# Performance work log

Hardware: AMD Instinct MI355X
Metric: run time of the kernel (lower is better)

Reference implementation:

```python
import jax, jax.numpy as jnp
import numpy as np

BS, Q, S1, S2 = 8, 128, 32, 64
H_DIM, NH = 768, 12
DH = H_DIM // NH


def _linear_params(k, scale=0.02):
    kw, _ = jax.random.split(k)
    w = jax.random.normal(kw, (H_DIM, H_DIM), jnp.float32) * scale
    b = jnp.zeros((H_DIM,), jnp.float32)
    return w, b


def setup_inputs() -> dict:
    root = jax.random.key(0)
    ks = jax.random.split(root, 12)
    wq_w, wq_b = _linear_params(ks[0])
    wk_w, wk_b = _linear_params(ks[1])
    wv_w, wv_b = _linear_params(ks[2])
    sq_w, sq_b = _linear_params(ks[3])
    sk_w, sk_b = _linear_params(ks[4])
    sv_w, sv_b = _linear_params(ks[5])
    return {
        "q_in": jax.random.normal(ks[6], (BS, Q, H_DIM), jnp.float32),
        "k_in": jax.random.normal(ks[7], (BS, S1, S2, H_DIM), jnp.float32),
        "v_in": jax.random.normal(ks[8], (BS, S1, S2, H_DIM), jnp.float32),
        "kvec": jax.random.normal(ks[9], (BS, S1, H_DIM), jnp.float32),
        "word_mask": jnp.ones((BS, S1, S2), jnp.int32),
        "sentence_mask": jnp.ones((BS * Q, S1), jnp.int32),
        "wq_w": wq_w, "wq_b": wq_b, "wk_w": wk_w, "wk_b": wk_b,
        "wv_w": wv_w, "wv_b": wv_b, "sq_w": sq_w, "sq_b": sq_b,
        "sk_w": sk_w, "sk_b": sk_b, "sv_w": sv_w, "sv_b": sv_b,
    }


def reference(q_in, k_in, v_in, kvec, word_mask, sentence_mask,
              wq_w, wq_b, wk_w, wk_b, wv_w, wv_b,
              sq_w, sq_b, sk_w, sk_b, sv_w, sv_b):
    bs, q_len = q_in.shape[0], q_in.shape[1]
    s1, s2 = k_in.shape[1], k_in.shape[2]
    scale = 1.0 / jnp.sqrt(jnp.float32(DH))

    # additive masks, as in the torch module
    wm = (1.0 - word_mask.astype(jnp.float32)) * -10000.0      # [bs, s1, s2]
    sm = (1.0 - sentence_mask.astype(jnp.float32)) * -10000.0  # [bs*Q, s1]

    # ---- word-level attention ----
    q = (q_in @ wq_w + wq_b).reshape(bs, q_len, NH, DH)
    k = (k_in @ wk_w + wk_b).reshape(bs, s1, s2, NH, DH)
    v = (v_in @ wv_w + wv_b).reshape(bs, s1, s2, NH, DH)
    # scores over tokens within each sentence: [bs, s1, H, Q, s2]
    scores1 = jnp.einsum('bqhd,bsthd->bshqt', q, k) * scale
    probs1 = jax.nn.softmax(scores1 + wm[:, :, None, None, :], axis=-1)
    # word_hidden: [bs, Q, s1, h]
    wh = jnp.einsum('bshqt,bsthd->bqshd', probs1, v).reshape(bs, q_len, s1, H_DIM)

    # ---- sentence-level attention ----
    sq = (q_in @ sq_w + sq_b).reshape(bs, q_len, NH, DH)
    sk = (kvec @ sk_w + sk_b).reshape(bs, s1, NH, DH)   # shared across queries
    sv = (wh @ sv_w + sv_b).reshape(bs, q_len, s1, NH, DH)
    scores2 = jnp.einsum('bqhd,bshd->bqhs', sq, sk) * scale  # [bs, Q, H, s1]
    scores2 = scores2 + sm.reshape(bs, q_len, s1)[:, :, None, :]
    probs2 = jax.nn.softmax(scores2, axis=-1)
    out = jnp.einsum('bqhs,bqshd->bqhd', probs2, sv).reshape(bs * q_len, H_DIM)
    return out
```

## Files before the change

### kernel.cpp

```cpp
#include <hip/hip_runtime.h>
#include <hip/hip_bf16.h>


typedef __attribute__((ext_vector_type(8))) short short8;
typedef __attribute__((ext_vector_type(4))) short short4v;
typedef __attribute__((ext_vector_type(4))) float f32x4;

__device__ __forceinline__ short f2bf(float f) {
  __hip_bfloat16 b = __float2bfloat16(f);
  return __builtin_bit_cast(short, b);
}
__device__ __forceinline__ float bf2f(short s) {
  __hip_bfloat16 b = __builtin_bit_cast(__hip_bfloat16, s);
  return __bfloat162float(b);
}

#define MFMA16(a, b, c) __builtin_amdgcn_mfma_f32_16x16x32_bf16((a), (b), (c), 0, 0, 0)

__device__ __forceinline__ void async_load16(const void* g, void* l) {
  auto l3 = (__attribute__((address_space(3))) void*)(uintptr_t)(
      reinterpret_cast<uintptr_t>(l));
  auto g1 = (const __attribute__((address_space(1))) void*)g;
  __builtin_amdgcn_global_load_lds(g1, l3, 16, 0, 0);
}

#define KBAR()                                      \
  do {                                              \
    asm volatile("" ::: "memory");                  \
    __builtin_amdgcn_s_barrier();                   \
    asm volatile("" ::: "memory");                  \
  } while (0)
#define VMW(N) asm volatile("s_waitcnt vmcnt(" #N ")" ::: "memory")

__global__ __launch_bounds__(256)
void prep(const float* __restrict__ w0, const float* __restrict__ w1,
          const float* __restrict__ w2, const float* __restrict__ w3,
          const float* __restrict__ w4, const float* __restrict__ w5,
          short* __restrict__ WT,
          const float* __restrict__ q_in, const float* __restrict__ k_in,
          const float* __restrict__ v_in, const float* __restrict__ kvec,
          short* __restrict__ qbf, short* __restrict__ kbf,
          short* __restrict__ vbf, short* __restrict__ kvb) {
  const int id = blockIdx.x;
  const int tid = threadIdx.x;
  if (id < 3456) {
    __shared__ float tile[32][33];
    const int zz = id / 576, r = id % 576;
    const float* W = (zz == 0) ? w0 : (zz == 1) ? w1 : (zz == 2) ? w2
                   : (zz == 3) ? w3 : (zz == 4) ? w4 : w5;
    short* WTo = WT + (size_t)zz * 768 * 768;
    const int bx = (r % 24) * 32, by = (r / 24) * 32;
    const int tx = tid & 31, ty = tid >> 5;
    #pragma unroll
    for (int i = 0; i < 32; i += 8)
      tile[ty + i][tx] = W[(size_t)(by + ty + i) * 768 + bx + tx];
    __syncthreads();
    #pragma unroll
    for (int i = 0; i < 32; i += 8)
      WTo[(size_t)(bx + ty + i) * 768 + by + tx] = f2bf(tile[tx][ty + i]);
    return;
  }
  const int i = (id - 3456) * 256 + tid;
  const float* src;
  short* dst;
  int idx;
  if (i < 98304)        { src = q_in; dst = qbf; idx = i; }
  else if (i < 1671168) { src = k_in; dst = kbf; idx = i - 98304; }
  else if (i < 3244032) { src = v_in; dst = vbf; idx = i - 1671168; }
  else                  { src = kvec; dst = kvb; idx = i - 3244032; }
  const float4* s = (const float4*)src + (size_t)idx * 2;
  const float4 a = s[0], b = s[1];
  __align__(16) short tmp[8] = {f2bf(a.x), f2bf(a.y), f2bf(a.z), f2bf(a.w),
                                f2bf(b.x), f2bf(b.y), f2bf(b.z), f2bf(b.w)};
  *((short8*)dst + idx) = *(short8*)tmp;
}

__global__ __launch_bounds__(512, 2)
void gemm_proj(const short* __restrict__ kbf, const short* __restrict__ vbf,
               const short* __restrict__ qbf, const short* __restrict__ kvb,
               const short* __restrict__ WT6,
               const float* __restrict__ wk_b, const float* __restrict__ wv_b,
               const float* __restrict__ wq_b, const float* __restrict__ sq_b,
               const float* __restrict__ sk_b,
               short* __restrict__ kp, short* __restrict__ vT,
               short* __restrict__ qp, float* __restrict__ sqp,
               float* __restrict__ skp) {
  const int K = 768, WELEM = 768 * 768;
  extern __shared__ __align__(16) char smem_c[];
  short* smem = (short*)smem_c;
  const int tid = threadIdx.x;
  const int w = tid >> 6, lane = tid & 63, quad = lane >> 4, l16 = lane & 15;
  const f32x4 zero4 = {0.f, 0.f, 0.f, 0.f};

  if (blockIdx.z < 2) {
    short* LA = smem;
    short* LB = smem + 2 * 256 * 64;
    const int z = blockIdx.z;
    const short* Ag = z ? vbf : kbf;
    const short* Bg = z ? (WT6 + 3 * WELEM) : (WT6 + 2 * WELEM);
    const float* bias = z ? wv_b : wk_b;
    const int m0 = blockIdx.x * 256, n0 = blockIdx.y * 256;
    const int wr = w >> 2, wc = w & 3;

    const int srow = lane >> 3;
    const int schk = (lane & 7) ^ srow;
    const short* ag0 = Ag + (size_t)(m0 + w * 8 + srow) * K + schk * 8;
    const short* bg0 = Bg + (size_t)(n0 + w * 8 + srow) * K + schk * 8;
    short* la0 = LA + (w * 8) * 64;
    short* lb0 = LB + (w * 8) * 64;
    const int fsw = l16 & 7;

    f32x4 acc[8][4];
    #pragma unroll
    for (int i = 0; i < 8; i++)
      #pragma unroll
      for (int j = 0; j < 4; j++) acc[i][j] = zero4;

    auto STG1 = [&](int op, int h, int kt) {
      if (kt >= 12) kt -= 2;
      const int buf = kt & 1;
      const short* g = (op ? bg0 : ag0) + (size_t)h * 128 * K + (size_t)kt * 64;
      short* lb = (op ? lb0 : la0) + buf * 16384 + h * (128 * 64);
      async_load16(g, lb);
      async_load16(g + (size_t)64 * K, lb + 64 * 64);
    };

    short8 af[4][2];
    short8 bf2[2][2];

#define LDA_(BUF, IH)                                                        \
  _Pragma("unroll") for (int i = 0; i < 4; i++)                              \
    _Pragma("unroll") for (int kb = 0; kb < 2; kb++)                         \
      af[i][kb] = *(const short8*)&LA[(BUF)*16384 +                          \
          (wr * 128 + (IH)*64 + i * 16 + l16) * 64 +                         \
          (((kb * 4 + quad) ^ fsw) * 8)];
#define LDB_(BUF, JH)                                                        \
  _Pragma("unroll") for (int j = 0; j < 2; j++)                              \
    _Pragma("unroll") for (int kb = 0; kb < 2; kb++)                         \
      bf2[j][kb] = *(const short8*)&LB[(BUF)*16384 +                         \
          (wc * 64 + (JH)*32 + j * 16 + l16) * 64 +                          \
          (((kb * 4 + quad) ^ fsw) * 8)];
#define MM_(IH, JH)                                                          \
  __builtin_amdgcn_s_setprio(1);                                             \
  _Pragma("unroll") for (int i = 0; i < 4; i++)                              \
    _Pragma("unroll") for (int j = 0; j < 2; j++) {                          \
      acc[(IH)*4 + i][(JH)*2 + j] =                                          \
          MFMA16(af[i][0], bf2[j][0], acc[(IH)*4 + i][(JH)*2 + j]);          \
      acc[(IH)*4 + i][(JH)*2 + j] =                                          \
          MFMA16(af[i][1], bf2[j][1], acc[(IH)*4 + i][(JH)*2 + j]);          \
    }                                                                        \
  __builtin_amdgcn_s_setprio(0);

    STG1(0, 0, 0); STG1(0, 1, 0); STG1(1, 0, 0); STG1(1, 1, 0);
    STG1(0, 0, 1);
    VMW(2);
    KBAR();

    #pragma unroll 1
    for (int it = 0; it < 6; ++it) {
      const int kb_t = 2 * it + 1, kc = 2 * it + 2, kd = 2 * it + 3;
      LDA_(0, 0); LDB_(0, 0); STG1(0, 1, kb_t); KBAR(); MM_(0, 0); KBAR();
      LDB_(0, 1); STG1(1, 0, kb_t); KBAR(); MM_(0, 1); KBAR();
      LDA_(0, 1); LDB_(0, 0); STG1(1, 1, kb_t); KBAR(); MM_(1, 0); KBAR();
      LDB_(0, 1); STG1(0, 0, kc); KBAR(); MM_(1, 1); VMW(2); KBAR();
      LDA_(1, 0); LDB_(1, 0); STG1(0, 1, kc); KBAR(); MM_(0, 0); KBAR();
      LDB_(1, 1); STG1(1, 0, kc); KBAR(); MM_(0, 1); KBAR();
      LDA_(1, 1); LDB_(1, 0); STG1(1, 1, kc); KBAR(); MM_(1, 0); KBAR();
      LDB_(1, 1); STG1(0, 0, kd); KBAR(); MM_(1, 1); VMW(2); KBAR();
    }
#undef LDA_
#undef LDB_
#undef MM_

    if (z == 0) {
      #pragma unroll
      for (int I = 0; I < 8; I++)
        #pragma unroll
        for (int J = 0; J < 4; J++) {
          const int col = n0 + wc * 64 + J * 16 + l16;
          const float bv = bias[col];
          #pragma unroll
          for (int r = 0; r < 4; r++) {
            const int g = m0 + wr * 128 + I * 16 + quad * 4 + r;
            kp[(size_t)g * 768 + col] = f2bf(acc[I][J][r] + bv);
          }
        }
    } else {
      const int hh = (n0 >> 6) + wc;
      #pragma unroll
      for (int I = 0; I < 8; I++) {
        const int bs_ = (m0 >> 6) + wr * 2 + (I >> 2);
        const int t0 = (I & 3) * 16 + quad * 4;
        #pragma unroll
        for (int J = 0; J < 4; J++) {
          const int dd = J * 16 + l16;
          const float bv = bias[hh * 64 + dd];
          __align__(8) short tmp[4];
          #pragma unroll
          for (int r = 0; r < 4; r++) tmp[r] = f2bf(acc[I][J][r] + bv);
          *(short4v*)&vT[(((size_t)bs_ * 12 + hh) * 64 + dd) * 64 + t0] =
              *(short4v*)tmp;
        }
      }
    }
    return;
  }

  {
    const int id = blockIdx.x + 64 * blockIdx.y;
    if (id >= 108) return;
    short* As = smem;
    short* Bs = smem + 128 * 32;
    const int qmode = (id < 96);
    const int r = qmode ? id : (id - 96);
    const int bx = qmode ? (r % 8) : (r % 2);
    const int by = qmode ? (r / 8) : (r / 2);
    const short* A = qmode ? qbf : kvb;
    const short* WT = qmode ? (WT6 + 0 * WELEM) : (WT6 + 4 * WELEM);

    const int wm = (w >> 1) * 64, wn = (w & 1) * 64;
    const int m0 = bx * 128, n0 = by * 128;
    const int grow = w * 32 + (lane >> 2);
    const int kc = (lane & 3) * 8;
    const short* ag = A + (size_t)(m0 + grow) * K + kc;
    const short* bg = WT + (size_t)(n0 + grow) * K + kc;
    short* al = &As[(w * 32) * 32];
    short* bl = &Bs[(w * 32) * 32];

    f32x4 acc[4][4];
    #pragma unroll
    for (int i = 0; i < 4; i++)
      #pragma unroll
      for (int j = 0; j < 4; j++) acc[i][j] = zero4;

    for (int k0 = 0; k0 < K; k0 += 32) {
      __syncthreads();
      if (tid < 256) {
        async_load16(ag, al);
        async_load16(ag + (size_t)16 * K, al + 16 * 32);
        async_load16(bg, bl);
        async_load16(bg + (size_t)16 * K, bl + 16 * 32);
      }
      ag += 32;
      bg += 32;
      __syncthreads();
      if (tid < 256) {
        short8 af[4], bf[4];
        #pragma unroll
        for (int i = 0; i < 4; i++)
          af[i] = *(short8*)&As[(wm + i * 16 + l16) * 32 + quad * 8];
        #pragma unroll
        for (int j = 0; j < 4; j++)
          bf[j] = *(short8*)&Bs[(wn + j * 16 + l16) * 32 + quad * 8];
        #pragma unroll
        for (int i = 0; i < 4; i++)
          #pragma unroll
          for (int j = 0; j < 4; j++)
            acc[i][j] = MFMA16(af[i], bf[j], acc[i][j]);
      }
    }
    if (tid >= 256) return;

    #pragma unroll
    for (int i = 0; i < 4; i++) {
      #pragma unroll
      for (int j = 0; j < 4; j++) {
        const int col = n0 + wn + j * 16 + l16;
        const float bv = qmode ? ((col < 768) ? wq_b[col] : sq_b[col - 768])
                               : sk_b[col];
        #pragma unroll
        for (int r4 = 0; r4 < 4; r4++) {
          const int g = m0 + wm + i * 16 + quad * 4 + r4;
          const float v = acc[i][j][r4] + bv;
          if (qmode) {
            if (col < 768) qp[(size_t)g * 768 + col] = f2bf(v * 0.125f);
            else sqp[(size_t)g * 768 + (col - 768)] = v;
          } else {
            skp[(size_t)g * 768 + col] = v;
          }
        }
      }
    }
  }
}

__global__ __launch_bounds__(256)
void wattn_sp(const short* __restrict__ q_proj, const short* __restrict__ k_proj,
              const short* __restrict__ vT, const int* __restrict__ word_mask,
              const float* __restrict__ sq, const float* __restrict__ sk,
              const int* __restrict__ sent_mask, short* __restrict__ wh,
              float* __restrict__ probs2) {
  __shared__ __align__(16) short KVs[128 * 72];
  __shared__ __align__(16) short Ps[128 * 72];
  const int bid = blockIdx.x;
  const int tid = threadIdx.x;

  if (bid >= 3072) {
    float* sc = (float*)KVs;
    const int bq = bid - 3072;
    const int b = bq >> 7, q = bq & 127;
    for (int p = tid; p < 384; p += 256) {
      const int hh = p >> 5, ss = p & 31;
      const float4* a = (const float4*)(sq + ((size_t)(b * 128 + q)) * 768 + hh * 64);
      const float4* c = (const float4*)(sk + ((size_t)(b * 32 + ss)) * 768 + hh * 64);
      float d = 0.f;
      #pragma unroll
      for (int i = 0; i < 16; i++) {
        const float4 av = a[i], cv = c[i];
        d += av.x * cv.x + av.y * cv.y + av.z * cv.z + av.w * cv.w;
      }
      d = d * 0.125f + (1.0f - (float)sent_mask[bq * 32 + ss]) * -10000.0f;
      sc[hh * 33 + ss] = d;
    }
    __syncthreads();
    if (tid < 12) {
      float mx = -3.0e38f;
      for (int ss = 0; ss < 32; ss++) mx = fmaxf(mx, sc[tid * 33 + ss]);
      float sum = 0.f;
      for (int ss = 0; ss < 32; ss++) {
        const float e = __expf(sc[tid * 33 + ss] - mx);
        sc[tid * 33 + ss] = e;
        sum += e;
      }
      const float inv = 1.0f / sum;
      for (int ss = 0; ss < 32; ss++) sc[tid * 33 + ss] *= inv;
    }
    __syncthreads();
    for (int p = tid; p < 384; p += 256) {
      const int hh = p >> 5, ss = p & 31;
      probs2[((size_t)bq * 12 + hh) * 32 + ss] = sc[hh * 33 + ss];
    }
    return;
  }

  short* Ks = KVs;
  short* Vs = KVs + 64 * 72;
  short* Os = KVs;
  const int h = bid % 12, s = (bid / 12) % 32, b = bid / (12 * 32);
  const int w = tid >> 6, lane = tid & 63, quad = lane >> 4, l16 = lane & 15;
  const f32x4 zero4 = {0.f, 0.f, 0.f, 0.f};

  {
    const int t2 = tid & 127;
    const int row8 = t2 >> 3;
    const int c8 = (t2 & 7) * 8;
    if (tid < 128) {
      const short* src = k_proj + ((size_t)((b * 32 + s) * 64)) * 768 + h * 64 + c8;
      #pragma unroll
      for (int i = 0; i < 4; i++) {
        const int r = row8 + i * 16;
        *(short8*)&Ks[r * 72 + c8] = *(const short8*)(src + (size_t)r * 768);
      }
    } else {
      const short* src = vT + ((size_t)((b * 32 + s) * 12 + h)) * 4096 + c8;
      #pragma unroll
      for (int i = 0; i < 4; i++) {
        const int r = row8 + i * 16;
        *(short8*)&Vs[r * 72 + c8] = *(const short8*)(src + (size_t)r * 64);
      }
    }
  }
  __syncthreads();

  f32x4 sac[2][4];
  #pragma unroll
  for (int i = 0; i < 2; i++)
    #pragma unroll
    for (int j = 0; j < 4; j++) sac[i][j] = zero4;
  {
    short8 aq[2][2], bk[4][2];
    #pragma unroll
    for (int i = 0; i < 2; i++)
      #pragma unroll
      for (int kb = 0; kb < 2; kb++)
        aq[i][kb] = *(const short8*)(q_proj +
            ((size_t)(b * 128 + w * 32 + i * 16 + l16)) * 768 + h * 64 + kb * 32 + quad * 8);
    #pragma unroll
    for (int j = 0; j < 4; j++)
      #pragma unroll
      for (int kb = 0; kb < 2; kb++)
        bk[j][kb] = *(short8*)&Ks[(j * 16 + l16) * 72 + kb * 32 + quad * 8];
    #pragma unroll
    for (int i = 0; i < 2; i++)
      #pragma unroll
      for (int j = 0; j < 4; j++) {
        sac[i][j] = MFMA16(aq[i][0], bk[j][0], sac[i][j]);
        sac[i][j] = MFMA16(aq[i][1], bk[j][1], sac[i][j]);
      }
  }

  {
    float wmv[4];
    const int* wmp = word_mask + (b * 32 + s) * 64;
    #pragma unroll
    for (int j = 0; j < 4; j++)
      wmv[j] = (1.0f - (float)wmp[j * 16 + l16]) * -10000.0f;
    #pragma unroll
    for (int i = 0; i < 2; i++) {
      #pragma unroll
      for (int r = 0; r < 4; r++) {
        float vv[4];
        float sum = 0.f;
        #pragma unroll
        for (int j = 0; j < 4; j++) {
          vv[j] = __expf(sac[i][j][r] + wmv[j]);
          sum += vv[j];
        }
        sum += __shfl_xor(sum, 1);
        sum += __shfl_xor(sum, 2);
        sum += __shfl_xor(sum, 4);
        sum += __shfl_xor(sum, 8);
        const float inv = 1.0f / sum;
        const int row = w * 32 + i * 16 + quad * 4 + r;
        #pragma unroll
        for (int j = 0; j < 4; j++)
          Ps[row * 72 + j * 16 + l16] = f2bf(vv[j] * inv);
      }
    }
  }
  __syncthreads();

  f32x4 oac[2][4];
  #pragma unroll
  for (int i = 0; i < 2; i++)
    #pragma unroll
    for (int j = 0; j < 4; j++) oac[i][j] = zero4;
  {
    short8 ap[2][2], bv[4][2];
    #pragma unroll
    for (int i = 0; i < 2; i++)
      #pragma unroll
      for (int kb = 0; kb < 2; kb++)
        ap[i][kb] = *(short8*)&Ps[(w * 32 + i * 16 + l16) * 72 + kb * 32 + quad * 8];
    #pragma unroll
    for (int j = 0; j < 4; j++)
      #pragma unroll
      for (int kb = 0; kb < 2; kb++)
        bv[j][kb] = *(short8*)&Vs[(j * 16 + l16) * 72 + kb * 32 + quad * 8];
    #pragma unroll
    for (int i = 0; i < 2; i++)
      #pragma unroll
      for (int j = 0; j < 4; j++) {
        oac[i][j] = MFMA16(ap[i][0], bv[j][0], oac[i][j]);
        oac[i][j] = MFMA16(ap[i][1], bv[j][1], oac[i][j]);
      }
  }
  __syncthreads();
  #pragma unroll
  for (int i = 0; i < 2; i++)
    #pragma unroll
    for (int j = 0; j < 4; j++)
      #pragma unroll
      for (int r = 0; r < 4; r++)
        Os[(w * 32 + i * 16 + quad * 4 + r) * 72 + j * 16 + l16] = f2bf(oac[i][j][r]);
  __syncthreads();

  {
    const int c8 = (tid & 7) * 8;
    #pragma unroll
    for (int i = 0; i < 4; i++) {
      const int row = i * 32 + (tid >> 3);
      short* dst = wh + (((size_t)(b * 128 + row)) * 32 + s) * 768 + h * 64;
      *(short8*)(dst + c8) = *(const short8*)&Os[row * 72 + c8];
    }
  }
}

__global__ __launch_bounds__(256)
void whc_kernel(const short* __restrict__ wh, const float* __restrict__ probs2,
                short* __restrict__ whc) {
  __shared__ __align__(16) short whs[32 * 776];
  __shared__ float p2s[384];
  const int bq = blockIdx.x, tid = threadIdx.x;
  const short8* src = (const short8*)(wh + (size_t)bq * 24576);
  for (int t = tid; t < 3072; t += 256) {
    const int row = t / 96, c8 = (t % 96) * 8;
    *(short8*)&whs[row * 776 + c8] = src[t];
  }
  for (int p = tid; p < 384; p += 256) p2s[p] = probs2[(size_t)bq * 384 + p];
  __syncthreads();

  float acc[3][12];
  #pragma unroll
  for (int kk = 0; kk < 3; kk++)
    #pragma unroll
    for (int h = 0; h < 12; h++) acc[kk][h] = 0.f;

  for (int s = 0; s < 32; s++) {
    float p2r[12];
    #pragma unroll
    for (int h = 0; h < 12; h++) p2r[h] = p2s[h * 32 + s];
    #pragma unroll
    for (int kk = 0; kk < 3; kk++) {
      const float wv = bf2f(whs[s * 776 + kk * 256 + tid]);
      #pragma unroll
      for (int h = 0; h < 12; h++) acc[kk][h] += p2r[h] * wv;
    }
  }
  #pragma unroll
  for (int h = 0; h < 12; h++)
    #pragma unroll
    for (int kk = 0; kk < 3; kk++)
      whc[((size_t)h * 1024 + bq) * 768 + kk * 256 + tid] = f2bf(acc[kk][h]);
}

__global__ __launch_bounds__(256)
void outg(const short* __restrict__ whc, const short* __restrict__ WTsv,
          const float* __restrict__ sv_b, float* __restrict__ out) {
  const int K = 768;
  __shared__ __align__(16) short As[128 * 32];
  __shared__ __align__(16) short Bs[64 * 32];
  const int tid = threadIdx.x;
  const int m0 = blockIdx.x * 128, h = blockIdx.y;
  const int w = tid >> 6, lane = tid & 63, quad = lane >> 4, l16 = lane & 15;
  const int wm = (w >> 1) * 64, wn = (w & 1) * 32;

  const int grow = w * 32 + (lane >> 2);
  const int kc = (lane & 3) * 8;
  const short* ag = whc + ((size_t)h * 1024 + m0 + grow) * K + kc;
  short* al = &As[(w * 32) * 32];
  const int growb = w * 16 + (lane >> 2);
  const short* bg = WTsv + (size_t)(h * 64 + growb) * K + kc;
  short* bl = &Bs[(w * 16) * 32];

  const f32x4 zero4 = {0.f, 0.f, 0.f, 0.f};
  f32x4 acc[4][2];
  #pragma unroll
  for (int i = 0; i < 4; i++)
    #pragma unroll
    for (int j = 0; j < 2; j++) acc[i][j] = zero4;

  for (int k0 = 0; k0 < K; k0 += 32) {
    __syncthreads();
    async_load16(ag, al);
    async_load16(ag + (size_t)16 * K, al + 16 * 32);
    async_load16(bg, bl);
    ag += 32;
    bg += 32;
    __syncthreads();
    short8 af[4], bf[2];
    #pragma unroll
    for (int i = 0; i < 4; i++)
      af[i] = *(short8*)&As[(wm + i * 16 + l16) * 32 + quad * 8];
    #pragma unroll
    for (int j = 0; j < 2; j++)
      bf[j] = *(short8*)&Bs[(wn + j * 16 + l16) * 32 + quad * 8];
    #pragma unroll
    for (int i = 0; i < 4; i++)
      #pragma unroll
      for (int j = 0; j < 2; j++)
        acc[i][j] = MFMA16(af[i], bf[j], acc[i][j]);
  }

  #pragma unroll
  for (int i = 0; i < 4; i++) {
    #pragma unroll
    for (int j = 0; j < 2; j++) {
      const int col = h * 64 + wn + j * 16 + l16;
      const float bv = sv_b[col];
      #pragma unroll
      for (int r = 0; r < 4; r++) {
        const int g = m0 + wm + i * 16 + quad * 4 + r;
        out[(size_t)g * 768 + col] = acc[i][j][r] + bv;
      }
    }
  }
}

extern "C" void kernel_launch(void* const* d_in, const int* in_sizes, int n_in,
                              void* d_out, int out_size, void* d_ws, size_t ws_size,
                              hipStream_t stream) {
  (void)in_sizes; (void)n_in; (void)out_size; (void)ws_size;
  const float* q_in      = (const float*)d_in[0];
  const float* k_in      = (const float*)d_in[1];
  const float* v_in      = (const float*)d_in[2];
  const float* kvec      = (const float*)d_in[3];
  const int*   word_mask = (const int*)d_in[4];
  const int*   sent_mask = (const int*)d_in[5];
  const float* wq_w = (const float*)d_in[6],  *wq_b = (const float*)d_in[7];
  const float* wk_w = (const float*)d_in[8],  *wk_b = (const float*)d_in[9];
  const float* wv_w = (const float*)d_in[10], *wv_b = (const float*)d_in[11];
  const float* sq_w = (const float*)d_in[12], *sq_b = (const float*)d_in[13];
  const float* sk_w = (const float*)d_in[14], *sk_b = (const float*)d_in[15];
  const float* sv_w = (const float*)d_in[16], *sv_b = (const float*)d_in[17];
  float* out = (float*)d_out;

  const int WELEM = 768 * 768;

  static bool s_attr_done = false;
  if (!s_attr_done) {
    (void)hipFuncSetAttribute(reinterpret_cast<const void*>(&gemm_proj),
                              hipFuncAttributeMaxDynamicSharedMemorySize, 131072);
    s_attr_done = true;
  }

  char* ws = (char*)d_ws;
  size_t off = 0;
  auto alloc = [&](size_t bytes) -> void* {
    void* p = ws + off;
    off += (bytes + 255) & ~(size_t)255;
    return p;
  };
  short* WT  = (short*)alloc((size_t)6 * 768 * 768 * 2);
  short* qbf = (short*)alloc((size_t)1024 * 768 * 2);
  short* kbf = (short*)alloc((size_t)16384 * 768 * 2);
  short* vbf = (short*)alloc((size_t)16384 * 768 * 2);
  short* kvb = (short*)alloc((size_t)256 * 768 * 2);
  short* qp  = (short*)alloc((size_t)1024 * 768 * 2);
  short* kp  = (short*)alloc((size_t)16384 * 768 * 2);
  short* vT  = (short*)alloc((size_t)16384 * 768 * 2);
  float* sqp = (float*)alloc((size_t)1024 * 768 * 4);
  float* skp = (float*)alloc((size_t)256 * 768 * 4);
  short* wh  = (short*)alloc((size_t)32768 * 768 * 2);
  float* pr2 = (float*)alloc((size_t)1024 * 12 * 32 * 4);
  short* whc = (short*)alloc((size_t)12 * 1024 * 768 * 2);

  prep<<<dim3(16224), 256, 0, stream>>>(wq_w, sq_w, wk_w, wv_w, sk_w, sv_w, WT,
                                        q_in, k_in, v_in, kvec, qbf, kbf, vbf, kvb);
  gemm_proj<<<dim3(64, 3, 3), 512, 131072, stream>>>(
      kbf, vbf, qbf, kvb, WT, wk_b, wv_b, wq_b, sq_b, sk_b,
      kp, vT, qp, sqp, skp);
  wattn_sp<<<dim3(4096), 256, 0, stream>>>(qp, kp, vT, word_mask, sqp, skp,
                                           sent_mask, wh, pr2);
  whc_kernel<<<dim3(1024), 256, 0, stream>>>(wh, pr2, whc);
  outg<<<dim3(8, 12), 256, 0, stream>>>(whc, WT + 5 * WELEM, sv_b, out);
}
```

Before: 317.8 us.

## Restructure K/V projection GEMM pipeline to keep both B halves in registers

The staging lambda now loads a whole 256-row A or B tile per call (four async loads) instead of half-tiles, and the B fragments for both column halves are kept in registers. Each phase therefore reloads B once per k-step rather than twice, and the MMA order becomes (0,0),(0,1),(1,1),(1,0). The global-to-LDS prefetch schedule is reorganized around this, with wait counts raised to 4 and a final drain added after the loop. This is meant to cut LDS reads and barrier-separated staging calls, at the cost of more registers and coarser-grained overlap.

Result: no change. 315.2 us (-0.8%).

```diff
diff --git a/kernel.cpp b/kernel.cpp
--- a/kernel.cpp
+++ b/kernel.cpp
@@ -116,17 +116,19 @@
       #pragma unroll
       for (int j = 0; j < 4; j++) acc[i][j] = zero4;
 
-    auto STG1 = [&](int op, int h, int kt) {
+    auto STG = [&](int op, int kt) {
       if (kt >= 12) kt -= 2;
       const int buf = kt & 1;
-      const short* g = (op ? bg0 : ag0) + (size_t)h * 128 * K + (size_t)kt * 64;
-      short* lb = (op ? lb0 : la0) + buf * 16384 + h * (128 * 64);
+      const short* g = (op ? bg0 : ag0) + (size_t)kt * 64;
+      short* lb = (op ? lb0 : la0) + buf * 16384;
       async_load16(g, lb);
       async_load16(g + (size_t)64 * K, lb + 64 * 64);
+      async_load16(g + (size_t)128 * K, lb + 128 * 64);
+      async_load16(g + (size_t)192 * K, lb + 192 * 64);
     };
 
     short8 af[4][2];
-    short8 bf2[2][2];
+    short8 bfr[2][2][2];
 
 #define LDA_(BUF, IH)                                                        \
   _Pragma("unroll") for (int i = 0; i < 4; i++)                              \
@@ -137,7 +139,7 @@
 #define LDB_(BUF, JH)                                                        \
   _Pragma("unroll") for (int j = 0; j < 2; j++)                              \
     _Pragma("unroll") for (int kb = 0; kb < 2; kb++)                         \
-      bf2[j][kb] = *(const short8*)&LB[(BUF)*16384 +                         \
+      bfr[JH][j][kb] = *(const short8*)&LB[(BUF)*16384 +                     \
           (wc * 64 + (JH)*32 + j * 16 + l16) * 64 +                          \
           (((kb * 4 + quad) ^ fsw) * 8)];
 #define MM_(IH, JH)                                                          \
@@ -145,32 +147,32 @@
   _Pragma("unroll") for (int i = 0; i < 4; i++)                              \
     _Pragma("unroll") for (int j = 0; j < 2; j++) {                          \
       acc[(IH)*4 + i][(JH)*2 + j] =                                          \
-          MFMA16(af[i][0], bf2[j][0], acc[(IH)*4 + i][(JH)*2 + j]);          \
+          MFMA16(af[i][0], bfr[JH][j][0], acc[(IH)*4 + i][(JH)*2 + j]);      \
       acc[(IH)*4 + i][(JH)*2 + j] =                                          \
-          MFMA16(af[i][1], bf2[j][1], acc[(IH)*4 + i][(JH)*2 + j]);          \
+          MFMA16(af[i][1], bfr[JH][j][1], acc[(IH)*4 + i][(JH)*2 + j]);      \
     }                                                                        \
   __builtin_amdgcn_s_setprio(0);
 
-    STG1(0, 0, 0); STG1(0, 1, 0); STG1(1, 0, 0); STG1(1, 1, 0);
-    STG1(0, 0, 1);
-    VMW(2);
+    STG(0, 0); STG(1, 0); STG(0, 1);
+    VMW(4);
     KBAR();
 
     #pragma unroll 1
     for (int it = 0; it < 6; ++it) {
-      const int kb_t = 2 * it + 1, kc = 2 * it + 2, kd = 2 * it + 3;
-      LDA_(0, 0); LDB_(0, 0); STG1(0, 1, kb_t); KBAR(); MM_(0, 0); KBAR();
-      LDB_(0, 1); STG1(1, 0, kb_t); KBAR(); MM_(0, 1); KBAR();
-      LDA_(0, 1); LDB_(0, 0); STG1(1, 1, kb_t); KBAR(); MM_(1, 0); KBAR();
-      LDB_(0, 1); STG1(0, 0, kc); KBAR(); MM_(1, 1); VMW(2); KBAR();
-      LDA_(1, 0); LDB_(1, 0); STG1(0, 1, kc); KBAR(); MM_(0, 0); KBAR();
-      LDB_(1, 1); STG1(1, 0, kc); KBAR(); MM_(0, 1); KBAR();
-      LDA_(1, 1); LDB_(1, 0); STG1(1, 1, kc); KBAR(); MM_(1, 0); KBAR();
-      LDB_(1, 1); STG1(0, 0, kd); KBAR(); MM_(1, 1); VMW(2); KBAR();
+      const int o = 2 * it + 1, e2 = 2 * it + 2, o2 = 2 * it + 3;
+      STG(1, o); LDA_(0, 0); LDB_(0, 0); KBAR(); MM_(0, 0); KBAR();
+      LDB_(0, 1); KBAR(); MM_(0, 1); KBAR();
+      LDA_(0, 1); KBAR(); MM_(1, 1); KBAR();
+      STG(0, e2); KBAR(); MM_(1, 0); VMW(4); KBAR();
+      STG(1, e2); LDA_(1, 0); LDB_(1, 0); KBAR(); MM_(0, 0); KBAR();
+      LDB_(1, 1); KBAR(); MM_(0, 1); KBAR();
+      LDA_(1, 1); KBAR(); MM_(1, 1); KBAR();
+      STG(0, o2); KBAR(); MM_(1, 0); VMW(4); KBAR();
     }
 #undef LDA_
 #undef LDB_
 #undef MM_
+    VMW(0);
 
     if (z == 0) {
       #pragma unroll
```

## Shrink K/V projection GEMM tile to 128x256 with simpler double-buffered pipeline

Applied to the files above, without the earlier changes.

The large K and V projection GEMM tile goes from 256x256 to 128x256 per block. The grid doubles along M and LDS use drops from 128KB to 96KB. The staging schedule is simplified to one k-tile per iteration with a full wait at each step, where before it streamed in halves with partial waits. This gives more blocks, better wave balance across CUs and fewer accumulator registers, at the cost of less reuse of the B operand per block and weaker load/compute overlap.

After: 332.7 us. +4.7%, slower.

```diff
diff --git a/kernel.cpp b/kernel.cpp
--- a/kernel.cpp
+++ b/kernel.cpp
@@ -94,12 +94,12 @@
 
   if (blockIdx.z < 2) {
     short* LA = smem;
-    short* LB = smem + 2 * 256 * 64;
+    short* LB = smem + 2 * 128 * 64;
     const int z = blockIdx.z;
     const short* Ag = z ? vbf : kbf;
     const short* Bg = z ? (WT6 + 3 * WELEM) : (WT6 + 2 * WELEM);
     const float* bias = z ? wv_b : wk_b;
-    const int m0 = blockIdx.x * 256, n0 = blockIdx.y * 256;
+    const int m0 = blockIdx.x * 128, n0 = blockIdx.y * 256;
     const int wr = w >> 2, wc = w & 3;
 
     const int srow = lane >> 3;
@@ -110,63 +110,62 @@
     short* lb0 = LB + (w * 8) * 64;
     const int fsw = l16 & 7;
 
-    f32x4 acc[8][4];
-    #pragma unroll
-    for (int i = 0; i < 8; i++)
+    f32x4 acc[4][4];
+    #pragma unroll
+    for (int i = 0; i < 4; i++)
       #pragma unroll
       for (int j = 0; j < 4; j++) acc[i][j] = zero4;
 
-    auto STG1 = [&](int op, int h, int kt) {
+    auto STGA = [&](int kt) {
       if (kt >= 12) kt -= 2;
       const int buf = kt & 1;
-      const short* g = (op ? bg0 : ag0) + (size_t)h * 128 * K + (size_t)kt * 64;
-      short* lb = (op ? lb0 : la0) + buf * 16384 + h * (128 * 64);
+      const short* g = ag0 + (size_t)kt * 64;
+      short* lb = la0 + buf * (128 * 64);
       async_load16(g, lb);
       async_load16(g + (size_t)64 * K, lb + 64 * 64);
     };
+    auto STGB = [&](int h, int kt) {
+      if (kt >= 12) kt -= 2;
+      const int buf = kt & 1;
+      const short* g = bg0 + (size_t)h * 128 * K + (size_t)kt * 64;
+      short* lb = lb0 + buf * (256 * 64) + h * (128 * 64);
+      async_load16(g, lb);
+      async_load16(g + (size_t)64 * K, lb + 64 * 64);
+    };
 
     short8 af[4][2];
-    short8 bf2[2][2];
-
-#define LDA_(BUF, IH)                                                        \
+    short8 bfr[2][2];
+
+#define LDA_(BUF)                                                            \
   _Pragma("unroll") for (int i = 0; i < 4; i++)                              \
     _Pragma("unroll") for (int kb = 0; kb < 2; kb++)                         \
-      af[i][kb] = *(const short8*)&LA[(BUF)*16384 +                          \
-          (wr * 128 + (IH)*64 + i * 16 + l16) * 64 +                         \
-          (((kb * 4 + quad) ^ fsw) * 8)];
+      af[i][kb] = *(const short8*)&LA[(BUF)*8192 +                           \
+          (wr * 64 + i * 16 + l16) * 64 + (((kb * 4 + quad) ^ fsw) * 8)];
 #define LDB_(BUF, JH)                                                        \
   _Pragma("unroll") for (int j = 0; j < 2; j++)                              \
     _Pragma("unroll") for (int kb = 0; kb < 2; kb++)                         \
-      bf2[j][kb] = *(const short8*)&LB[(BUF)*16384 +                         \
+      bfr[j][kb] = *(const short8*)&LB[(BUF)*16384 +                         \
           (wc * 64 + (JH)*32 + j * 16 + l16) * 64 +                          \
           (((kb * 4 + quad) ^ fsw) * 8)];
-#define MM_(IH, JH)                                                          \
+#define MM_(JH)                                                              \
   __builtin_amdgcn_s_setprio(1);                                             \
   _Pragma("unroll") for (int i = 0; i < 4; i++)                              \
     _Pragma("unroll") for (int j = 0; j < 2; j++) {                          \
-      acc[(IH)*4 + i][(JH)*2 + j] =                                          \
-          MFMA16(af[i][0], bf2[j][0], acc[(IH)*4 + i][(JH)*2 + j]);          \
-      acc[(IH)*4 + i][(JH)*2 + j] =                                          \
-          MFMA16(af[i][1], bf2[j][1], acc[(IH)*4 + i][(JH)*2 + j]);          \
+      acc[i][(JH)*2 + j] = MFMA16(af[i][0], bfr[j][0], acc[i][(JH)*2 + j]);  \
+      acc[i][(JH)*2 + j] = MFMA16(af[i][1], bfr[j][1], acc[i][(JH)*2 + j]);  \
     }                                                                        \
   __builtin_amdgcn_s_setprio(0);
 
-    STG1(0, 0, 0); STG1(0, 1, 0); STG1(1, 0, 0); STG1(1, 1, 0);
-    STG1(0, 0, 1);
-    VMW(2);
-    KBAR();
+    STGA(0); STGB(0, 0); STGB(1, 0);
+    VMW(0); KBAR();
 
     #pragma unroll 1
-    for (int it = 0; it < 6; ++it) {
-      const int kb_t = 2 * it + 1, kc = 2 * it + 2, kd = 2 * it + 3;
-      LDA_(0, 0); LDB_(0, 0); STG1(0, 1, kb_t); KBAR(); MM_(0, 0); KBAR();
-      LDB_(0, 1); STG1(1, 0, kb_t); KBAR(); MM_(0, 1); KBAR();
-      LDA_(0, 1); LDB_(0, 0); STG1(1, 1, kb_t); KBAR(); MM_(1, 0); KBAR();
-      LDB_(0, 1); STG1(0, 0, kc); KBAR(); MM_(1, 1); VMW(2); KBAR();
-      LDA_(1, 0); LDB_(1, 0); STG1(0, 1, kc); KBAR(); MM_(0, 0); KBAR();
-      LDB_(1, 1); STG1(1, 0, kc); KBAR(); MM_(0, 1); KBAR();
-      LDA_(1, 1); LDB_(1, 0); STG1(1, 1, kc); KBAR(); MM_(1, 0); KBAR();
-      LDB_(1, 1); STG1(0, 0, kd); KBAR(); MM_(1, 1); VMW(2); KBAR();
+    for (int t = 0; t < 12; ++t) {
+      const int c = t & 1;
+      LDA_(c); LDB_(c, 0); STGA(t + 1); STGB(0, t + 1);
+      KBAR(); MM_(0); KBAR();
+      LDB_(c, 1); STGB(1, t + 1);
+      KBAR(); MM_(1); VMW(0); KBAR();
     }
 #undef LDA_
 #undef LDB_
@@ -174,23 +173,23 @@
 
     if (z == 0) {
       #pragma unroll
-      for (int I = 0; I < 8; I++)
+      for (int I = 0; I < 4; I++)
         #pragma unroll
         for (int J = 0; J < 4; J++) {
           const int col = n0 + wc * 64 + J * 16 + l16;
           const float bv = bias[col];
           #pragma unroll
           for (int r = 0; r < 4; r++) {
-            const int g = m0 + wr * 128 + I * 16 + quad * 4 + r;
+            const int g = m0 + wr * 64 + I * 16 + quad * 4 + r;
             kp[(size_t)g * 768 + col] = f2bf(acc[I][J][r] + bv);
           }
         }
     } else {
       const int hh = (n0 >> 6) + wc;
-      #pragma unroll
-      for (int I = 0; I < 8; I++) {
-        const int bs_ = (m0 >> 6) + wr * 2 + (I >> 2);
-        const int t0 = (I & 3) * 16 + quad * 4;
+      const int bs_ = (m0 >> 6) + wr;
+      #pragma unroll
+      for (int I = 0; I < 4; I++) {
+        const int t0 = I * 16 + quad * 4;
         #pragma unroll
         for (int J = 0; J < 4; J++) {
           const int dd = J * 16 + l16;
@@ -207,7 +206,7 @@
   }
 
   {
-    const int id = blockIdx.x + 64 * blockIdx.y;
+    const int id = blockIdx.x + 128 * blockIdx.y;
     if (id >= 108) return;
     short* As = smem;
     short* Bs = smem + 128 * 32;
@@ -590,7 +589,7 @@
   static bool s_attr_done = false;
   if (!s_attr_done) {
     (void)hipFuncSetAttribute(reinterpret_cast<const void*>(&gemm_proj),
-                              hipFuncAttributeMaxDynamicSharedMemorySize, 131072);
+                              hipFuncAttributeMaxDynamicSharedMemorySize, 98304);
     s_attr_done = true;
   }
 
@@ -617,7 +616,7 @@
 
   prep<<<dim3(16224), 256, 0, stream>>>(wq_w, sq_w, wk_w, wv_w, sk_w, sv_w, WT,
                                         q_in, k_in, v_in, kvec, qbf, kbf, vbf, kvb);
-  gemm_proj<<<dim3(64, 3, 3), 512, 131072, stream>>>(
+  gemm_proj<<<dim3(128, 3, 3), 512, 98304, stream>>>(
       kbf, vbf, qbf, kvb, WT, wk_b, wv_b, wq_b, sq_b, sk_b,
       kp, vT, qp, sqp, skp);
   wattn_sp<<<dim3(4096), 256, 0, stream>>>(qp, kp, vT, word_mask, sqp, skp,
```
